# Performance work log

Hardware: AMD Instinct MI355X
Metric: run time of the kernel (lower is better)

## Reference

```python
import jax, jax.numpy as jnp
import numpy as np

NUM_HEADS = 16
NEG_INF = -2.0**32 + 1.0  # matches torch code's padding value
LN_EPS = 1e-5


def setup_inputs() -> dict:
    key = jax.random.key(0)
    ks = jax.random.split(key, 4)
    B, S, D = 8, 1024, 1024
    x = jax.random.normal(ks[0], (B, S, D), dtype=jnp.float32)
    W_qkv = jax.random.normal(ks[1], (D, 3 * D), dtype=jnp.float32) * 0.02
    b_qkv = jnp.zeros((3 * D,), dtype=jnp.float32)
    W_out = jax.random.normal(ks[2], (D, D), dtype=jnp.float32) * 0.02
    b_out = jnp.zeros((D,), dtype=jnp.float32)
    gamma = jnp.ones((D,), dtype=jnp.float32)
    beta = jnp.zeros((D,), dtype=jnp.float32)
    return {"x": x, "W_qkv": W_qkv, "b_qkv": b_qkv, "W_out": W_out,
            "b_out": b_out, "gamma": gamma, "beta": beta}


def reference(x, W_qkv, b_qkv, W_out, b_out, gamma, beta):
    B, S, D = x.shape
    H = NUM_HEADS
    hd = D // H
    # fused QKV projection
    qkv = x @ W_qkv + b_qkv                      # [B, S, 3D]
    q, k, v = jnp.split(qkv, 3, axis=-1)         # each [B, S, D]
    # split heads: chunk along feature dim == reshape to [B, H, S, hd]
    q = q.reshape(B, S, H, hd).transpose(0, 2, 1, 3)
    k = k.reshape(B, S, H, hd).transpose(0, 2, 1, 3)
    v = v.reshape(B, S, H, hd).transpose(0, 2, 1, 3)
    # NOTE: original scales by sqrt(num_units), not sqrt(head_dim)
    scale = jnp.float32(1.0 / (D ** 0.5))
    scores = jnp.einsum('bhqd,bhkd->bhqk', q, k) * scale   # [B, H, S, S]
    causal = jnp.tril(jnp.ones((S, S), dtype=bool))
    scores = jnp.where(causal, scores, jnp.float32(NEG_INF))
    attn = jax.nn.softmax(scores, axis=-1)
    o = jnp.einsum('bhqk,bhkd->bhqd', attn, v)             # [B, H, S, hd]
    o = o.transpose(0, 2, 1, 3).reshape(B, S, D)           # concat heads
    out = o @ W_out + b_out + x                            # proj + residual
    # LayerNorm over last dim
    mu = jnp.mean(out, axis=-1, keepdims=True)
    var = jnp.mean((out - mu) ** 2, axis=-1, keepdims=True)
    out = (out - mu) * jax.lax.rsqrt(var + LN_EPS) * gamma + beta
    return out
```

## Files before the change

kernel.cpp:

```cpp
#include <hip/hip_runtime.h>
#include <math.h>

typedef __attribute__((ext_vector_type(8))) short bf16x8;
typedef __attribute__((ext_vector_type(4))) float f32x4;

#define DEV __device__ __forceinline__

DEV unsigned short f2b(float f) {
    union { float f; unsigned u; } x;
    x.f = f;
    unsigned r = x.u + 0x7fff + ((x.u >> 16) & 1);
    return (unsigned short)(r >> 16);
}
DEV float b2f(unsigned short u) {
    union { unsigned u; float f; } x;
    x.u = ((unsigned)u) << 16;
    return x.f;
}

DEV void glds16(const void* g, void* l) {
    __builtin_amdgcn_global_load_lds(
        (const __attribute__((address_space(1))) void*)g,
        (__attribute__((address_space(3))) void*)l, 16, 0, 0);
}

__global__ __launch_bounds__(256) void cvt_bf16(
    const float* __restrict__ in, unsigned short* __restrict__ out)
{
    int i = (blockIdx.x * 256 + threadIdx.x) * 8;
    float4 a = *(const float4*)(in + i);
    float4 b = *(const float4*)(in + i + 4);
    int4 tv;
    short* tp = reinterpret_cast<short*>(&tv);
    tp[0] = (short)f2b(a.x); tp[1] = (short)f2b(a.y);
    tp[2] = (short)f2b(a.z); tp[3] = (short)f2b(a.w);
    tp[4] = (short)f2b(b.x); tp[5] = (short)f2b(b.y);
    tp[6] = (short)f2b(b.z); tp[7] = (short)f2b(b.w);
    *(int4*)(out + i) = tv;
}

__global__ __launch_bounds__(256) void transpose_cvt(
    const float* __restrict__ W, unsigned short* __restrict__ Wt, int N)
{
    __shared__ short S[64 * 65];
    const int n0 = blockIdx.x * 64, k0 = blockIdx.y * 64;
    const int tid = threadIdx.x;
#pragma unroll
    for (int p = 0; p < 16; p++) {
        int idx = p * 256 + tid;
        int r = idx >> 6, c = idx & 63;
        S[c * 65 + r] = (short)f2b(W[(size_t)(k0 + r) * N + n0 + c]);
    }
    __syncthreads();
#pragma unroll
    for (int p = 0; p < 8; p++) {
        int idx = p * 256 + tid;
        int r = idx >> 5, cp = (idx & 31) * 2;
        unsigned lo = (unsigned short)S[r * 65 + cp];
        unsigned hi = (unsigned short)S[r * 65 + cp + 1];
        *(unsigned*)(Wt + (size_t)(n0 + r) * 1024 + k0 + cp) = lo | (hi << 16);
    }
}

__global__ __launch_bounds__(256) void qkv_gemm(
    const unsigned short* __restrict__ Xb,
    const unsigned short* __restrict__ Wt,
    const float* __restrict__ bq,
    unsigned short* __restrict__ Qb,
    unsigned short* __restrict__ Kf,
    unsigned short* __restrict__ Vf)
{
    __shared__ __align__(16) short Sh[128 * 64 * 2];
    short* As = Sh;
    short* Bs = Sh + 8192;

    const int flat = blockIdx.y * 24 + blockIdx.x;
    const int xcd = flat & 7, local = flat >> 3;
    const int m0 = (xcd * 8 + local / 24) * 128;
    const int n0 = (local % 24) * 128;

    const int tid = threadIdx.x;
    const int wave = tid >> 6, lane = tid & 63;
    const int quad = lane >> 4, lcol = lane & 15;
    const int wrow = (wave >> 1) * 64, wcol = (wave & 1) * 64;

    f32x4 acc[4][4];
#pragma unroll
    for (int i = 0; i < 4; i++)
#pragma unroll
        for (int j = 0; j < 4; j++) acc[i][j] = (f32x4){0.f, 0.f, 0.f, 0.f};

    const int sr = tid >> 3;
    const int g_lin = tid & 7;
    const int g_src = g_lin ^ (sr & 7);
    const int swz = lcol & 7;

    for (int k0 = 0; k0 < 1024; k0 += 64) {
        __syncthreads();
#pragma unroll
        for (int p = 0; p < 4; p++) {
            glds16(Xb + (size_t)(m0 + p * 32 + sr) * 1024 + k0 + g_src * 8,
                   &As[(p * 32 + sr) * 64 + g_lin * 8]);
            glds16(Wt + (size_t)(n0 + p * 32 + sr) * 1024 + k0 + g_src * 8,
                   &Bs[(p * 32 + sr) * 64 + g_lin * 8]);
        }
        __syncthreads();
#pragma unroll
        for (int kk = 0; kk < 2; kk++) {
            bf16x8 a[4], b[4];
#pragma unroll
            for (int i = 0; i < 4; i++)
                a[i] = *(const bf16x8*)(&As[(wrow + 16 * i + lcol) * 64
                                            + ((kk * 4 + quad) ^ swz) * 8]);
#pragma unroll
            for (int j = 0; j < 4; j++)
                b[j] = *(const bf16x8*)(&Bs[(wcol + 16 * j + lcol) * 64
                                            + ((kk * 4 + quad) ^ swz) * 8]);
#pragma unroll
            for (int i = 0; i < 4; i++)
#pragma unroll
                for (int j = 0; j < 4; j++)
                    acc[i][j] = __builtin_amdgcn_mfma_f32_16x16x32_bf16(
                        a[i], b[j], acc[i][j], 0, 0, 0);
        }
    }
    __syncthreads();

    short* Es = Sh;
    const int which = n0 >> 10;
    const int h0 = (n0 & 1023) >> 6;
    const int bb = m0 >> 10;
    const int sl0 = m0 & 1023;
    const int kt = sl0 >> 7;

#pragma unroll
    for (int j = 0; j < 4; j++) {
        int colt = wcol + 16 * j + lcol;
        float bias = bq[n0 + colt];
        int g = colt >> 6, e = colt & 63;
#pragma unroll
        for (int i = 0; i < 4; i++) {
#pragma unroll
            for (int reg = 0; reg < 4; reg++) {
                int ls = wrow + 16 * i + quad * 4 + reg;
                unsigned short v = f2b(acc[i][j][reg] + bias);
                int off;
                if (which == 0)
                    off = ls * 64 + e;
                else if (which == 1)
                    off = (e >> 5) * 4096 + (ls >> 4) * 512
                        + (((e >> 3) & 3) * 16 + (ls & 15)) * 8 + (e & 7);
                else
                    off = (ls >> 5) * 2048 + (e >> 4) * 512
                        + (((ls >> 3) & 3) * 16 + (e & 15)) * 8 + (ls & 7);
                Es[g * 8192 + off] = (short)v;
            }
        }
    }
    __syncthreads();

#pragma unroll
    for (int rd = 0; rd < 8; rd++) {
        int fl = rd * 2048 + tid * 8;
        int g = fl >> 13, off = fl & 8191;
        bf16x8 val = *(const bf16x8*)(&Es[fl]);
        int bh = bb * 16 + h0 + g;
        if (which == 0)
            *(bf16x8*)(Qb + ((size_t)bh * 1024 + sl0) * 64 + off) = val;
        else if (which == 1)
            *(bf16x8*)(Kf + ((size_t)bh * 8 + kt) * 8192 + off) = val;
        else
            *(bf16x8*)(Vf + ((size_t)bh * 8 + kt) * 8192 + off) = val;
    }
}

__global__ __launch_bounds__(256, 4) void attn_kern(
    const unsigned short* __restrict__ Qb,
    const unsigned short* __restrict__ Kf,
    const unsigned short* __restrict__ Vf,
    unsigned short* __restrict__ Ob)
{
    __shared__ __align__(16) short Ps[64 * 136];

    const int xb = blockIdx.x;
    const int bh = blockIdx.y;
    const int pr = xb >> 1;
    const int hf = xb & 1;
    const unsigned short* Qp = Qb + (size_t)bh * 65536;
    const unsigned short* Kp = Kf + (size_t)bh * 65536;
    const unsigned short* Vp = Vf + (size_t)bh * 65536;

    const int tid = threadIdx.x;
    const int wave = tid >> 6, lane = tid & 63;
    const int quad = lane >> 4, lcol = lane & 15;
    const int hw4 = hf * 4 + wave;
    const int qloc = hw4 * 16 + lcol;

    const float sc2 = 0.0450711882f;
    const int b = bh >> 4, h = bh & 15;

    for (int pass = 0; pass < 2; pass++) {
        const int qt = pass ? (7 - pr) : pr;
        const int q0 = qt * 128 + hf * 64 + wave * 16;

        bf16x8 qa[2];
#pragma unroll
        for (int kk = 0; kk < 2; kk++)
            qa[kk] = *(const bf16x8*)(Qp + (size_t)(q0 + lcol) * 64
                                      + kk * 32 + quad * 8);

        f32x4 o_acc[4];
#pragma unroll
        for (int jo = 0; jo < 4; jo++) o_acc[jo] = (f32x4){0.f, 0.f, 0.f, 0.f};
        float l_loc = 0.f;

        for (int kt = 0; kt <= qt; kt++) {
            const bool diag = (kt == qt);
            const int jmax = diag ? hw4 : 7;
            const int kk2max = diag ? (hw4 >> 1) : 3;

            f32x4 scT[8];
#pragma unroll
            for (int j = 0; j < 8; j++) scT[j] = (f32x4){0.f, 0.f, 0.f, 0.f};
#pragma unroll
            for (int kk = 0; kk < 2; kk++) {
                bf16x8 kb[8];
#pragma unroll
                for (int j = 0; j < 8; j++)
                    if (j <= jmax)
                        kb[j] = *(const bf16x8*)(Kp
                            + ((size_t)((kt * 2 + kk) * 8 + j) << 9) + lane * 8);
#pragma unroll
                for (int j = 0; j < 8; j++)
                    if (j <= jmax)
                        scT[j] = __builtin_amdgcn_mfma_f32_16x16x32_bf16(
                            kb[j], qa[kk], scT[j], 0, 0, 0);
            }

#pragma unroll
            for (int j = 0; j < 8; j++) {
                if (j <= jmax) {
                    float pv[4];
#pragma unroll
                    for (int r = 0; r < 4; r++) {
                        float p = exp2f(scT[j][r] * sc2);
                        if (diag && (16 * j + quad * 4 + r) > qloc) p = 0.f;
                        l_loc += p;
                        pv[r] = p;
                    }
                    ushort4 pk;
                    pk.x = f2b(pv[0]); pk.y = f2b(pv[1]);
                    pk.z = f2b(pv[2]); pk.w = f2b(pv[3]);
                    *(ushort4*)(&Ps[(wave * 16 + lcol) * 136 + 16 * j + quad * 4]) = pk;
                }
            }
            if (diag && !(jmax & 1)) {
                *(ushort4*)(&Ps[(wave * 16 + lcol) * 136 + 16 * (jmax + 1) + quad * 4]) =
                    (ushort4){0, 0, 0, 0};
            }

#pragma unroll
            for (int kk2 = 0; kk2 < 4; kk2++) {
                if (kk2 <= kk2max) {
                    bf16x8 pa = *(const bf16x8*)(&Ps[(wave * 16 + lcol) * 136
                                                     + kk2 * 32 + quad * 8]);
                    bf16x8 vb[4];
#pragma unroll
                    for (int jo = 0; jo < 4; jo++)
                        vb[jo] = *(const bf16x8*)(Vp
                            + ((size_t)((kt * 4 + kk2) * 4 + jo) << 9) + lane * 8);
#pragma unroll
                    for (int jo = 0; jo < 4; jo++)
                        o_acc[jo] = __builtin_amdgcn_mfma_f32_16x16x32_bf16(
                            pa, vb[jo], o_acc[jo], 0, 0, 0);
                }
            }
        }

        l_loc += __shfl_xor(l_loc, 16);
        l_loc += __shfl_xor(l_loc, 32);
        float inv = 1.0f / l_loc;
        float invq[4];
#pragma unroll
        for (int r = 0; r < 4; r++) invq[r] = __shfl(inv, quad * 4 + r);

#pragma unroll
        for (int jo = 0; jo < 4; jo++) {
#pragma unroll
            for (int r = 0; r < 4; r++) {
                int q = q0 + quad * 4 + r;
                Ob[(size_t)(b * 1024 + q) * 1024 + h * 64 + 16 * jo + lcol] =
                    f2b(o_acc[jo][r] * invq[r]);
            }
        }
        l_loc = 0.f;
    }
}

__global__ __launch_bounds__(256) void out_gemm(
    const unsigned short* __restrict__ O,
    const unsigned short* __restrict__ Wt2,
    const float* __restrict__ bo,
    const float* __restrict__ X,
    unsigned short* __restrict__ P2)
{
    __shared__ __align__(16) short As[128 * 64];
    __shared__ __align__(16) short Bs[128 * 64];

    const int flat = blockIdx.y * 8 + blockIdx.x;
    const int xcd = flat & 7, local = flat >> 3;
    const int m0 = (xcd * 8 + (local >> 3)) * 128;
    const int n0 = (local & 7) * 128;

    const int tid = threadIdx.x;
    const int wave = tid >> 6, lane = tid & 63;
    const int quad = lane >> 4, lcol = lane & 15;
    const int wrow = (wave >> 1) * 64, wcol = (wave & 1) * 64;

    f32x4 acc[4][4];
#pragma unroll
    for (int i = 0; i < 4; i++)
#pragma unroll
        for (int j = 0; j < 4; j++) acc[i][j] = (f32x4){0.f, 0.f, 0.f, 0.f};

    const int sr = tid >> 3;
    const int g_lin = tid & 7;
    const int g_src = g_lin ^ (sr & 7);
    const int swz = lcol & 7;

    for (int k0 = 0; k0 < 1024; k0 += 64) {
        __syncthreads();
#pragma unroll
        for (int p = 0; p < 4; p++) {
            glds16(O + (size_t)(m0 + p * 32 + sr) * 1024 + k0 + g_src * 8,
                   &As[(p * 32 + sr) * 64 + g_lin * 8]);
            glds16(Wt2 + (size_t)(n0 + p * 32 + sr) * 1024 + k0 + g_src * 8,
                   &Bs[(p * 32 + sr) * 64 + g_lin * 8]);
        }
        __syncthreads();
#pragma unroll
        for (int kk = 0; kk < 2; kk++) {
            bf16x8 a[4], b[4];
#pragma unroll
            for (int i = 0; i < 4; i++)
                a[i] = *(const bf16x8*)(&As[(wrow + 16 * i + lcol) * 64
                                            + ((kk * 4 + quad) ^ swz) * 8]);
#pragma unroll
            for (int j = 0; j < 4; j++)
                b[j] = *(const bf16x8*)(&Bs[(wcol + 16 * j + lcol) * 64
                                            + ((kk * 4 + quad) ^ swz) * 8]);
#pragma unroll
            for (int i = 0; i < 4; i++)
#pragma unroll
                for (int j = 0; j < 4; j++)
                    acc[i][j] = __builtin_amdgcn_mfma_f32_16x16x32_bf16(
                        a[i], b[j], acc[i][j], 0, 0, 0);
        }
    }

#pragma unroll
    for (int j = 0; j < 4; j++) {
        int c = n0 + wcol + 16 * j + lcol;
        float bias = bo[c];
#pragma unroll
        for (int i = 0; i < 4; i++) {
#pragma unroll
            for (int reg = 0; reg < 4; reg++) {
                int r = m0 + wrow + 16 * i + quad * 4 + reg;
                float v = acc[i][j][reg] + bias + X[(size_t)r * 1024 + c];
                P2[(size_t)r * 1024 + c] = f2b(v);
            }
        }
    }
}

__global__ __launch_bounds__(256) void ln_kern(
    const unsigned short* __restrict__ P2,
    const float* __restrict__ G,
    const float* __restrict__ Bt,
    float* __restrict__ out)
{
    const int row = blockIdx.x, tid = threadIdx.x;
    const size_t base = (size_t)row * 1024 + tid * 4;

    int2 raw = *(const int2*)(P2 + base);
    float v[4];
    v[0] = b2f((unsigned short)(raw.x & 0xffff));
    v[1] = b2f((unsigned short)((unsigned)raw.x >> 16));
    v[2] = b2f((unsigned short)(raw.y & 0xffff));
    v[3] = b2f((unsigned short)((unsigned)raw.y >> 16));

    float sum = v[0] + v[1] + v[2] + v[3];
    float sq = v[0] * v[0] + v[1] * v[1] + v[2] * v[2] + v[3] * v[3];
#pragma unroll
    for (int m = 1; m < 64; m <<= 1) {
        sum += __shfl_xor(sum, m);
        sq += __shfl_xor(sq, m);
    }
    __shared__ float rs[4], rq[4];
    const int wave = tid >> 6, lane = tid & 63;
    if (lane == 0) { rs[wave] = sum; rq[wave] = sq; }
    __syncthreads();
    sum = rs[0] + rs[1] + rs[2] + rs[3];
    sq = rq[0] + rq[1] + rq[2] + rq[3];

    float mean = sum * (1.0f / 1024.0f);
    float var = fmaxf(sq * (1.0f / 1024.0f) - mean * mean, 0.0f);
    float rstd = rsqrtf(var + 1e-5f);

    float4 g = *(const float4*)(G + tid * 4);
    float4 be = *(const float4*)(Bt + tid * 4);

    float4 o;
    o.x = (v[0] - mean) * rstd * g.x + be.x;
    o.y = (v[1] - mean) * rstd * g.y + be.y;
    o.z = (v[2] - mean) * rstd * g.z + be.z;
    o.w = (v[3] - mean) * rstd * g.w + be.w;
    *(float4*)(out + base) = o;
}

extern "C" void kernel_launch(void* const* d_in, const int* in_sizes, int n_in,
                              void* d_out, int out_size, void* d_ws, size_t ws_size,
                              hipStream_t stream) {
    const float* x    = (const float*)d_in[0];
    const float* Wqkv = (const float*)d_in[1];
    const float* bqkv = (const float*)d_in[2];
    const float* Wout = (const float*)d_in[3];
    const float* bout = (const float*)d_in[4];
    const float* gam  = (const float*)d_in[5];
    const float* bet  = (const float*)d_in[6];
    float* out = (float*)d_out;

    char* ws = (char*)d_ws;
    const size_t MB = (size_t)1024 * 1024;

    unsigned short* Qb  = (unsigned short*)d_out;
    unsigned short* Ob  = (unsigned short*)d_out + 8388608;
    unsigned short* Kf  = (unsigned short*)(ws);
    unsigned short* Vf  = (unsigned short*)(ws + 16 * MB);
    unsigned short* Wt2 = (unsigned short*)(ws + 32 * MB);
    unsigned short* Xb  = (unsigned short*)(ws + 34 * MB);
    unsigned short* Wt  = (unsigned short*)(ws + 50 * MB);
    unsigned short* P2  = (unsigned short*)(ws + 34 * MB);

    cvt_bf16<<<4096, 256, 0, stream>>>(x, Xb);
    transpose_cvt<<<dim3(48, 16), 256, 0, stream>>>(Wqkv, Wt, 3072);
    transpose_cvt<<<dim3(16, 16), 256, 0, stream>>>(Wout, Wt2, 1024);
    qkv_gemm<<<dim3(24, 64), 256, 0, stream>>>(Xb, Wt, bqkv, Qb, Kf, Vf);
    attn_kern<<<dim3(8, 128), 256, 0, stream>>>(Qb, Kf, Vf, Ob);
    out_gemm<<<dim3(8, 64), 256, 0, stream>>>(Ob, Wt2, bout, x, P2);
    ln_kern<<<8192, 256, 0, stream>>>(P2, gam, bet, out);
}
```

Before: 271.7 us.

## Double-buffer LDS in QKV and output GEMMs, make QKV blocks persistent over three N tiles

Both GEMM kernels now use two LDS stages, so the global-to-LDS loads for the next K slice are issued before the MFMA work on the current slice, with one barrier per iteration instead of two. The QKV GEMM launches 512 blocks, each looping over three 128-wide N tiles for a fixed M tile. This cuts the launch count and lets the X rows be reused from cache. Doubling LDS to 64KB per block may lower occupancy, and the persistent loop serializes work that previously ran on separate blocks.

```diff
diff --git a/kernel.cpp b/kernel.cpp
--- a/kernel.cpp
+++ b/kernel.cpp
@@ -70,107 +70,125 @@
     unsigned short* __restrict__ Kf,
     unsigned short* __restrict__ Vf)
 {
-    __shared__ __align__(16) short Sh[128 * 64 * 2];
-    short* As = Sh;
-    short* Bs = Sh + 8192;
-
-    const int flat = blockIdx.y * 24 + blockIdx.x;
+    __shared__ __align__(16) short Sh[2][16384];
+
+    const int flat = blockIdx.x;
     const int xcd = flat & 7, local = flat >> 3;
-    const int m0 = (xcd * 8 + local / 24) * 128;
-    const int n0 = (local % 24) * 128;
+    const int m0 = (xcd * 8 + (local >> 3)) * 128;
+    const int ng = local & 7;
 
     const int tid = threadIdx.x;
     const int wave = tid >> 6, lane = tid & 63;
     const int quad = lane >> 4, lcol = lane & 15;
     const int wrow = (wave >> 1) * 64, wcol = (wave & 1) * 64;
 
-    f32x4 acc[4][4];
-#pragma unroll
-    for (int i = 0; i < 4; i++)
-#pragma unroll
-        for (int j = 0; j < 4; j++) acc[i][j] = (f32x4){0.f, 0.f, 0.f, 0.f};
-
     const int sr = tid >> 3;
     const int g_lin = tid & 7;
     const int g_src = g_lin ^ (sr & 7);
     const int swz = lcol & 7;
 
-    for (int k0 = 0; k0 < 1024; k0 += 64) {
-        __syncthreads();
-#pragma unroll
-        for (int p = 0; p < 4; p++) {
-            glds16(Xb + (size_t)(m0 + p * 32 + sr) * 1024 + k0 + g_src * 8,
-                   &As[(p * 32 + sr) * 64 + g_lin * 8]);
-            glds16(Wt + (size_t)(n0 + p * 32 + sr) * 1024 + k0 + g_src * 8,
-                   &Bs[(p * 32 + sr) * 64 + g_lin * 8]);
-        }
-        __syncthreads();
-#pragma unroll
-        for (int kk = 0; kk < 2; kk++) {
-            bf16x8 a[4], b[4];
-#pragma unroll
-            for (int i = 0; i < 4; i++)
-                a[i] = *(const bf16x8*)(&As[(wrow + 16 * i + lcol) * 64
-                                            + ((kk * 4 + quad) ^ swz) * 8]);
-#pragma unroll
-            for (int j = 0; j < 4; j++)
-                b[j] = *(const bf16x8*)(&Bs[(wcol + 16 * j + lcol) * 64
-                                            + ((kk * 4 + quad) ^ swz) * 8]);
-#pragma unroll
-            for (int i = 0; i < 4; i++)
-#pragma unroll
-                for (int j = 0; j < 4; j++)
-                    acc[i][j] = __builtin_amdgcn_mfma_f32_16x16x32_bf16(
-                        a[i], b[j], acc[i][j], 0, 0, 0);
-        }
-    }
-    __syncthreads();
-
-    short* Es = Sh;
-    const int which = n0 >> 10;
-    const int h0 = (n0 & 1023) >> 6;
     const int bb = m0 >> 10;
     const int sl0 = m0 & 1023;
     const int kt = sl0 >> 7;
 
-#pragma unroll
-    for (int j = 0; j < 4; j++) {
-        int colt = wcol + 16 * j + lcol;
-        float bias = bq[n0 + colt];
-        int g = colt >> 6, e = colt & 63;
-#pragma unroll
-        for (int i = 0; i < 4; i++) {
-#pragma unroll
-            for (int reg = 0; reg < 4; reg++) {
-                int ls = wrow + 16 * i + quad * 4 + reg;
-                unsigned short v = f2b(acc[i][j][reg] + bias);
-                int off;
-                if (which == 0)
-                    off = ls * 64 + e;
-                else if (which == 1)
-                    off = (e >> 5) * 4096 + (ls >> 4) * 512
-                        + (((e >> 3) & 3) * 16 + (ls & 15)) * 8 + (e & 7);
-                else
-                    off = (ls >> 5) * 2048 + (e >> 4) * 512
-                        + (((ls >> 3) & 3) * 16 + (e & 15)) * 8 + (ls & 7);
-                Es[g * 8192 + off] = (short)v;
-            }
-        }
-    }
-    __syncthreads();
-
-#pragma unroll
-    for (int rd = 0; rd < 8; rd++) {
-        int fl = rd * 2048 + tid * 8;
-        int g = fl >> 13, off = fl & 8191;
-        bf16x8 val = *(const bf16x8*)(&Es[fl]);
-        int bh = bb * 16 + h0 + g;
-        if (which == 0)
-            *(bf16x8*)(Qb + ((size_t)bh * 1024 + sl0) * 64 + off) = val;
-        else if (which == 1)
-            *(bf16x8*)(Kf + ((size_t)bh * 8 + kt) * 8192 + off) = val;
-        else
-            *(bf16x8*)(Vf + ((size_t)bh * 8 + kt) * 8192 + off) = val;
+    for (int tt = 0; tt < 3; tt++) {
+        const int n0 = (ng * 3 + tt) * 128;
+
+        f32x4 acc[4][4];
+#pragma unroll
+        for (int i = 0; i < 4; i++)
+#pragma unroll
+            for (int j = 0; j < 4; j++) acc[i][j] = (f32x4){0.f, 0.f, 0.f, 0.f};
+
+#pragma unroll
+        for (int p = 0; p < 4; p++) {
+            glds16(Xb + (size_t)(m0 + p * 32 + sr) * 1024 + 0 + g_src * 8,
+                   &Sh[0][(p * 32 + sr) * 64 + g_lin * 8]);
+            glds16(Wt + (size_t)(n0 + p * 32 + sr) * 1024 + 0 + g_src * 8,
+                   &Sh[0][8192 + (p * 32 + sr) * 64 + g_lin * 8]);
+        }
+        __syncthreads();
+
+        int cur = 0;
+        for (int ks = 0; ks < 16; ks++) {
+            if (ks < 15) {
+                const int k1 = (ks + 1) * 64;
+#pragma unroll
+                for (int p = 0; p < 4; p++) {
+                    glds16(Xb + (size_t)(m0 + p * 32 + sr) * 1024 + k1 + g_src * 8,
+                           &Sh[cur ^ 1][(p * 32 + sr) * 64 + g_lin * 8]);
+                    glds16(Wt + (size_t)(n0 + p * 32 + sr) * 1024 + k1 + g_src * 8,
+                           &Sh[cur ^ 1][8192 + (p * 32 + sr) * 64 + g_lin * 8]);
+                }
+            }
+            const short* As = &Sh[cur][0];
+            const short* Bs = &Sh[cur][8192];
+#pragma unroll
+            for (int kk = 0; kk < 2; kk++) {
+                bf16x8 a[4], b[4];
+#pragma unroll
+                for (int i = 0; i < 4; i++)
+                    a[i] = *(const bf16x8*)(&As[(wrow + 16 * i + lcol) * 64
+                                                + ((kk * 4 + quad) ^ swz) * 8]);
+#pragma unroll
+                for (int j = 0; j < 4; j++)
+                    b[j] = *(const bf16x8*)(&Bs[(wcol + 16 * j + lcol) * 64
+                                                + ((kk * 4 + quad) ^ swz) * 8]);
+#pragma unroll
+                for (int i = 0; i < 4; i++)
+#pragma unroll
+                    for (int j = 0; j < 4; j++)
+                        acc[i][j] = __builtin_amdgcn_mfma_f32_16x16x32_bf16(
+                            a[i], b[j], acc[i][j], 0, 0, 0);
+            }
+            __syncthreads();
+            cur ^= 1;
+        }
+
+        short* Es = &Sh[0][0];
+        const int which = n0 >> 10;
+        const int h0 = (n0 & 1023) >> 6;
+
+#pragma unroll
+        for (int j = 0; j < 4; j++) {
+            int colt = wcol + 16 * j + lcol;
+            float bias = bq[n0 + colt];
+            int g = colt >> 6, e = colt & 63;
+#pragma unroll
+            for (int i = 0; i < 4; i++) {
+#pragma unroll
+                for (int reg = 0; reg < 4; reg++) {
+                    int ls = wrow + 16 * i + quad * 4 + reg;
+                    unsigned short v = f2b(acc[i][j][reg] + bias);
+                    int off;
+                    if (which == 0)
+                        off = ls * 64 + e;
+                    else if (which == 1)
+                        off = (e >> 5) * 4096 + (ls >> 4) * 512
+                            + (((e >> 3) & 3) * 16 + (ls & 15)) * 8 + (e & 7);
+                    else
+                        off = (ls >> 5) * 2048 + (e >> 4) * 512
+                            + (((ls >> 3) & 3) * 16 + (e & 15)) * 8 + (ls & 7);
+                    Es[g * 8192 + off] = (short)v;
+                }
+            }
+        }
+        __syncthreads();
+
+#pragma unroll
+        for (int rd = 0; rd < 8; rd++) {
+            int fl = rd * 2048 + tid * 8;
+            int g = fl >> 13, off = fl & 8191;
+            bf16x8 val = *(const bf16x8*)(&Es[fl]);
+            int bh = bb * 16 + h0 + g;
+            if (which == 0)
+                *(bf16x8*)(Qb + ((size_t)bh * 1024 + sl0) * 64 + off) = val;
+            else if (which == 1)
+                *(bf16x8*)(Kf + ((size_t)bh * 8 + kt) * 8192 + off) = val;
+            else
+                *(bf16x8*)(Vf + ((size_t)bh * 8 + kt) * 8192 + off) = val;
+        }
+        __syncthreads();
     }
 }
 
@@ -304,8 +322,7 @@
     const float* __restrict__ X,
     unsigned short* __restrict__ P2)
 {
-    __shared__ __align__(16) short As[128 * 64];
-    __shared__ __align__(16) short Bs[128 * 64];
+    __shared__ __align__(16) short Sh[2][16384];
 
     const int flat = blockIdx.y * 8 + blockIdx.x;
     const int xcd = flat & 7, local = flat >> 3;
@@ -328,16 +345,29 @@
     const int g_src = g_lin ^ (sr & 7);
     const int swz = lcol & 7;
 
-    for (int k0 = 0; k0 < 1024; k0 += 64) {
-        __syncthreads();
-#pragma unroll
-        for (int p = 0; p < 4; p++) {
-            glds16(O + (size_t)(m0 + p * 32 + sr) * 1024 + k0 + g_src * 8,
-                   &As[(p * 32 + sr) * 64 + g_lin * 8]);
-            glds16(Wt2 + (size_t)(n0 + p * 32 + sr) * 1024 + k0 + g_src * 8,
-                   &Bs[(p * 32 + sr) * 64 + g_lin * 8]);
-        }
-        __syncthreads();
+#pragma unroll
+    for (int p = 0; p < 4; p++) {
+        glds16(O + (size_t)(m0 + p * 32 + sr) * 1024 + 0 + g_src * 8,
+               &Sh[0][(p * 32 + sr) * 64 + g_lin * 8]);
+        glds16(Wt2 + (size_t)(n0 + p * 32 + sr) * 1024 + 0 + g_src * 8,
+               &Sh[0][8192 + (p * 32 + sr) * 64 + g_lin * 8]);
+    }
+    __syncthreads();
+
+    int cur = 0;
+    for (int ks = 0; ks < 16; ks++) {
+        if (ks < 15) {
+            const int k1 = (ks + 1) * 64;
+#pragma unroll
+            for (int p = 0; p < 4; p++) {
+                glds16(O + (size_t)(m0 + p * 32 + sr) * 1024 + k1 + g_src * 8,
+                       &Sh[cur ^ 1][(p * 32 + sr) * 64 + g_lin * 8]);
+                glds16(Wt2 + (size_t)(n0 + p * 32 + sr) * 1024 + k1 + g_src * 8,
+                       &Sh[cur ^ 1][8192 + (p * 32 + sr) * 64 + g_lin * 8]);
+            }
+        }
+        const short* As = &Sh[cur][0];
+        const short* Bs = &Sh[cur][8192];
 #pragma unroll
         for (int kk = 0; kk < 2; kk++) {
             bf16x8 a[4], b[4];
@@ -356,6 +386,8 @@
                     acc[i][j] = __builtin_amdgcn_mfma_f32_16x16x32_bf16(
                         a[i], b[j], acc[i][j], 0, 0, 0);
         }
+        __syncthreads();
+        cur ^= 1;
     }
 
 #pragma unroll
@@ -446,7 +478,7 @@
     cvt_bf16<<<4096, 256, 0, stream>>>(x, Xb);
     transpose_cvt<<<dim3(48, 16), 256, 0, stream>>>(Wqkv, Wt, 3072);
     transpose_cvt<<<dim3(16, 16), 256, 0, stream>>>(Wout, Wt2, 1024);
-    qkv_gemm<<<dim3(24, 64), 256, 0, stream>>>(Xb, Wt, bqkv, Qb, Kf, Vf);
+    qkv_gemm<<<512, 256, 0, stream>>>(Xb, Wt, bqkv, Qb, Kf, Vf);
     attn_kern<<<dim3(8, 128), 256, 0, stream>>>(Qb, Kf, Vf, Ob);
     out_gemm<<<dim3(8, 64), 256, 0, stream>>>(Ob, Wt2, bout, x, P2);
     ln_kern<<<8192, 256, 0, stream>>>(P2, gam, bet, out);
```

New measurement: 281.3 us. +3.5%, slower.
